# Kernel tuning notes

Hardware: AMD Instinct MI355X
Metric: run time of the kernel (lower is better)

Reference implementation:

```python
import jax, jax.numpy as jnp
import numpy as np

N_NODES = 4096
NUM_GRAPHS = 16
NODE_DIM = 8
EDGE_DIM = 4
HID = 128
N_WIRES = 9  # 3 edge wires + 4 node wires (center=3) + 2 ancillas
SEL_LAYERS = 1
PI = np.pi


def _c(x):
    return x.astype(jnp.complex64)


def _ry(t):
    c, s = _c(jnp.cos(t / 2)), _c(jnp.sin(t / 2))
    return jnp.stack([jnp.stack([c, -s], -1), jnp.stack([s, c], -1)], -2)


def _rx(t):
    c, s = _c(jnp.cos(t / 2)), -1j * _c(jnp.sin(t / 2))
    return jnp.stack([jnp.stack([c, s], -1), jnp.stack([s, c], -1)], -2)


def _rz(t):
    e = jnp.exp(-0.5j * _c(t))
    z = jnp.zeros_like(e)
    return jnp.stack([jnp.stack([e, z], -1), jnp.stack([z, jnp.conj(e)], -1)], -2)


def _rot(phi, theta, omega):  # qml.Rot = RZ(omega) @ RY(theta) @ RZ(phi)
    return _rz(omega) @ _ry(theta) @ _rz(phi)


def _ctrl(U):  # block-diag(I2, U)
    b = U.shape[:-2]
    I = jnp.broadcast_to(jnp.eye(2, dtype=jnp.complex64), b + (2, 2))
    Z = jnp.zeros(b + (2, 2), jnp.complex64)
    return jnp.concatenate([jnp.concatenate([I, Z], -1), jnp.concatenate([Z, U], -1)], -2)


_CNOT = jnp.array([[1, 0, 0, 0], [0, 1, 0, 0], [0, 0, 0, 1], [0, 0, 1, 0]], jnp.complex64)


def _apply1(state, U, w):  # state [S, 2**9], U [2,2] or [S,2,2]
    S = state.shape[0]
    s = jnp.moveaxis(state.reshape((S,) + (2,) * N_WIRES), 1 + w, 1)
    out = jnp.einsum('bij,bjk->bik', jnp.broadcast_to(U, (S, 2, 2)), s.reshape(S, 2, -1))
    return jnp.moveaxis(out.reshape(s.shape), 1, 1 + w).reshape(S, -1)


def _apply2(state, U, w1, w2):  # U [4,4] or [S,4,4], wire order (w1,w2)
    S = state.shape[0]
    s = jnp.moveaxis(state.reshape((S,) + (2,) * N_WIRES), (1 + w1, 1 + w2), (1, 2))
    out = jnp.einsum('bij,bjk->bik', jnp.broadcast_to(U, (S, 4, 4)), s.reshape(S, 4, -1))
    return jnp.moveaxis(out.reshape(s.shape), (1, 2), (1 + w1, 1 + w2)).reshape(S, -1)


def _sel(state, weights, wires):  # qml.StronglyEntanglingLayers, weights [L, n, 3]->here [L,3,3]
    L, n = weights.shape[0], len(wires)
    for l in range(L):
        for j, w in enumerate(wires):
            state = _apply1(state, _rot(weights[l, j, 0], weights[l, j, 1], weights[l, j, 2]), w)
        r = l % (n - 1) + 1
        for j in range(n):
            state = _apply2(state, _CNOT, wires[j], wires[(j + r) % n])
    return state


def _pqc(inputs, strong, inits, update):
    # inputs: [S, 7, 2] angles (rows 0..2 edge feats, rows 3..6 node feats, center node = row 3)
    S = inputs.shape[0]
    state = jnp.zeros((S, 2 ** N_WIRES), jnp.complex64).at[:, 0].set(1.0)
    for i in range(3):
        state = _apply1(state, _ry(inputs[:, i, 0]), i)
        state = _apply1(state, _rz(inputs[:, i, 1]), i)
    for i in range(4):
        state = _apply1(state, _ry(inputs[:, 3 + i, 0]), 3 + i)
        state = _apply1(state, _rz(inputs[:, 3 + i, 1]), 3 + i)
    for i in range(3):  # message_passing_pqc per edge
        e, nb, a1, a2 = i, 4 + i, 7, 8
        state = _apply2(state, _ctrl(_rx(inits[0, 0])), nb, a1)
        state = _apply2(state, _ctrl(_ry(inits[0, 1])), e, a1)
        state = _apply2(state, _ctrl(_rz(inits[0, 2])), nb, a2)
        state = _apply2(state, _ctrl(_ry(inits[0, 3])), e, a2)
        state = _sel(state, strong[0], [e, nb, a1])
        state = _sel(state, strong[1], [a1, nb, a2])
    state = _sel(state, update, [3, 7, 8])
    # expval(PauliX) on center wire 3: wires 0..2 -> 8, wire 3 -> 2, wires 4..8 -> 32
    s = state.reshape(S, 8, 2, 32)
    return 2.0 * jnp.real(jnp.sum(jnp.conj(s[:, :, 0]) * s[:, :, 1], axis=(1, 2)))


def _mlp(x, W1, b1, W2, b2):  # PyG MLP, act between layers, dropout in eval = identity
    return jax.nn.leaky_relu(x @ W1 + b1) @ W2 + b2


def _forward(node_feat, edge_attr, Wn1, bn1, Wn2, bn2, We1, be1, We2, be2,
             strong, inits, update, Wu1, bu1, Wu2, bu2, Wh1, bh1, Wh2, bh2,
             subgraphs, edge_ids, batch):
    x = jnp.tanh(_mlp(node_feat, Wn1, bn1, Wn2, bn2)) * PI   # input_process
    e = jnp.tanh(_mlp(edge_attr, We1, be1, We2, be2)) * PI
    q_in = jnp.concatenate([e[edge_ids], x[subgraphs]], axis=1)  # [S,3,2]+[S,4,2] -> [S,7,2]
    aggr = _pqc(q_in, strong, inits, update)[:, None]            # [S,1]
    centers = subgraphs[:, 0]
    upd = _mlp(jnp.concatenate([x[centers], aggr], axis=-1), Wu1, bu1, Wu2, bu2)  # [S,2]
    x = x + jnp.zeros_like(x).at[centers].add(upd)               # index_add + residual
    gsum = jax.ops.segment_sum(x, batch, num_segments=NUM_GRAPHS)
    gcnt = jax.ops.segment_sum(jnp.ones((x.shape[0], 1), x.dtype), batch, num_segments=NUM_GRAPHS)
    g = gsum / gcnt                                              # global_mean_pool
    return _mlp(g, Wh1, bh1, Wh2, bh2)


def setup_inputs() -> dict:
    key = jax.random.key(0)
    ks = jax.random.split(key, 16)
    N, G = N_NODES, NUM_GRAPHS
    node_feat = jax.random.normal(ks[0], (N, NODE_DIM), jnp.float32)
    edge_attr = jax.random.normal(ks[1], (3 * N, EDGE_DIM), jnp.float32)
    i = np.arange(N)
    # star subgraph per node: center i with ring neighbors i+1,i+2,i+3 (mod N);
    # edge (i, i+k) has id 3*i + (k-1) in edge_attr (idx_dict materialized).
    subgraphs = jnp.asarray(np.stack([i, (i + 1) % N, (i + 2) % N, (i + 3) % N], 1), jnp.int32)
    edge_ids = jnp.asarray(np.stack([3 * i, 3 * i + 1, 3 * i + 2], 1), jnp.int32)
    batch = jnp.asarray(i // (N // G), jnp.int32)

    def lin(k, fan_in, shape):
        return jax.random.uniform(k, shape, jnp.float32, -1.0, 1.0) / np.sqrt(fan_in)

    def qw(k, shape):  # uniform_pi_init
        return jax.random.uniform(k, shape, jnp.float32, 0.0, PI)

    k = jax.random.split(ks[2], 24)
    return {
        'node_feat': node_feat, 'edge_attr': edge_attr,
        'Wn1': lin(k[0], NODE_DIM, (NODE_DIM, HID)), 'bn1': lin(k[1], NODE_DIM, (HID,)),
        'Wn2': lin(k[2], HID, (HID, 2)), 'bn2': lin(k[3], HID, (2,)),
        'We1': lin(k[4], EDGE_DIM, (EDGE_DIM, HID)), 'be1': lin(k[5], EDGE_DIM, (HID,)),
        'We2': lin(k[6], HID, (HID, 2)), 'be2': lin(k[7], HID, (2,)),
        'strong': qw(k[8], (2, SEL_LAYERS, 3, 3)), 'inits': qw(k[9], (1, 4)),
        'update': qw(k[10], (SEL_LAYERS, 3, 3)),
        'Wu1': lin(k[11], 3, (3, HID)), 'bu1': lin(k[12], 3, (HID,)),
        'Wu2': lin(k[13], HID, (HID, 2)), 'bu2': lin(k[14], HID, (2,)),
        'Wh1': lin(k[15], 2, (2, 2)), 'bh1': lin(k[16], 2, (2,)),
        'Wh2': lin(k[17], 2, (2, 2)), 'bh2': lin(k[18], 2, (2,)),
        'subgraphs': subgraphs, 'edge_ids': edge_ids, 'batch': batch,
    }


def reference(node_feat, edge_attr, Wn1, bn1, Wn2, bn2, We1, be1, We2, be2,
              strong, inits, update, Wu1, bu1, Wu2, bu2, Wh1, bh1, Wh2, bh2,
              subgraphs, edge_ids, batch):
    return _forward(node_feat, edge_attr, Wn1, bn1, Wn2, bn2, We1, be1, We2, be2,
                    strong, inits, update, Wu1, bu1, Wu2, bu2, Wh1, bh1, Wh2, bh2,
                    subgraphs, edge_ids, batch)
```

## Files before the change

### kernel.cpp

```cpp
#include <hip/hip_runtime.h>
#include <math.h>

#define PI_F 3.14159265358979323846f

__device__ __forceinline__ float2 cmul2(float2 a, float2 b) {
    return make_float2(a.x * b.x - a.y * b.y, a.x * b.y + a.y * b.x);
}
__device__ __forceinline__ float2 cmac2(float2 u, float2 a, float2 v, float2 b) {
    float2 r;
    r.x = u.x * a.x - u.y * a.y + v.x * b.x - v.y * b.y;
    r.y = u.x * a.y + u.y * a.x + v.x * b.y + v.y * b.x;
    return r;
}

struct M4 { float2 u00, u01, u10, u11; };

__device__ __forceinline__ M4 mmul4(const M4& A, const M4& B) {
    M4 R;
    R.u00 = cmac2(A.u00, B.u00, A.u01, B.u10);
    R.u01 = cmac2(A.u00, B.u01, A.u01, B.u11);
    R.u10 = cmac2(A.u10, B.u00, A.u11, B.u10);
    R.u11 = cmac2(A.u10, B.u01, A.u11, B.u11);
    return R;
}
__device__ __forceinline__ M4 mry(float t) {
    float c = cosf(0.5f * t), s = sinf(0.5f * t);
    M4 R; R.u00 = {c, 0}; R.u01 = {-s, 0}; R.u10 = {s, 0}; R.u11 = {c, 0};
    return R;
}
__device__ __forceinline__ M4 mrz(float t) {
    float c = cosf(0.5f * t), s = sinf(0.5f * t);
    M4 R; R.u00 = {c, -s}; R.u01 = {0, 0}; R.u10 = {0, 0}; R.u11 = {c, s};
    return R;
}
__device__ __forceinline__ M4 mrot(float phi, float th, float om) {
    return mmul4(mmul4(mrz(om), mry(th)), mrz(phi));
}

__device__ __forceinline__ float2 shflx(float2 v, int mask) {
    return make_float2(__shfl_xor(v.x, mask, 64), __shfl_xor(v.y, mask, 64));
}

__device__ __forceinline__ M4 ldm(const float* __restrict__ g) {
    M4 M;
    M.u00 = make_float2(g[0], g[1]); M.u01 = make_float2(g[2], g[3]);
    M.u10 = make_float2(g[4], g[5]); M.u11 = make_float2(g[6], g[7]);
    return M;
}


template <int TB>
__device__ __forceinline__ void rot_reg(const M4& U, float2 (&amp)[8]) {
#pragma unroll
    for (int r = 0; r < 8; r++)
        if (((r >> TB) & 1) == 0) {
            int r1 = r | (1 << TB);
            float2 a = amp[r], b = amp[r1];
            amp[r]  = cmac2(U.u00, a, U.u01, b);
            amp[r1] = cmac2(U.u10, a, U.u11, b);
        }
}

template <int LB>
__device__ __forceinline__ void rot_lane(const M4& U, float2 (&amp)[8], int lane) {
    bool hi = (lane >> LB) & 1;
    float2 cA = hi ? U.u11 : U.u00;
    float2 cB = hi ? U.u10 : U.u01;
#pragma unroll
    for (int r = 0; r < 8; r++) {
        float2 o = shflx(amp[r], 1 << LB);
        amp[r] = cmac2(cA, amp[r], cB, o);
    }
}

template <int WIRE>
__device__ __forceinline__ void rot1(const M4& U, float2 (&amp)[8], int lane) {
    constexpr int BIT = 8 - WIRE;
    if constexpr (BIT < 3) rot_reg<BIT>(U, amp);
    else rot_lane<BIT - 3>(U, amp, lane);
}


template <int CBIT, int TB>
__device__ __forceinline__ void crx_g(float c, float s, float2 (&amp)[8], int lane) {
    if constexpr (CBIT >= 3) {
        bool ct = (lane >> (CBIT - 3)) & 1;
        float cc = ct ? c : 1.f, ss = ct ? s : 0.f;
#pragma unroll
        for (int r = 0; r < 8; r++)
            if (((r >> TB) & 1) == 0) {
                int r1 = r | (1 << TB);
                float2 a = amp[r], b = amp[r1];
                amp[r]  = make_float2(cc * a.x + ss * b.y, cc * a.y - ss * b.x);
                amp[r1] = make_float2(ss * a.y + cc * b.x, cc * b.y - ss * a.x);
            }
    } else {
#pragma unroll
        for (int r = 0; r < 8; r++)
            if (((r >> CBIT) & 1) == 1 && ((r >> TB) & 1) == 0) {
                int r1 = r | (1 << TB);
                float2 a = amp[r], b = amp[r1];
                amp[r]  = make_float2(c * a.x + s * b.y, c * a.y - s * b.x);
                amp[r1] = make_float2(s * a.y + c * b.x, c * b.y - s * a.x);
            }
    }
}

template <int CBIT, int TB>
__device__ __forceinline__ void cry_g(float c, float s, float2 (&amp)[8], int lane) {
    if constexpr (CBIT >= 3) {
        bool ct = (lane >> (CBIT - 3)) & 1;
        float cc = ct ? c : 1.f, ss = ct ? s : 0.f;
#pragma unroll
        for (int r = 0; r < 8; r++)
            if (((r >> TB) & 1) == 0) {
                int r1 = r | (1 << TB);
                float2 a = amp[r], b = amp[r1];
                amp[r]  = make_float2(cc * a.x - ss * b.x, cc * a.y - ss * b.y);
                amp[r1] = make_float2(ss * a.x + cc * b.x, ss * a.y + cc * b.y);
            }
    } else {
#pragma unroll
        for (int r = 0; r < 8; r++)
            if (((r >> CBIT) & 1) == 1 && ((r >> TB) & 1) == 0) {
                int r1 = r | (1 << TB);
                float2 a = amp[r], b = amp[r1];
                amp[r]  = make_float2(c * a.x - s * b.x, c * a.y - s * b.y);
                amp[r1] = make_float2(s * a.x + c * b.x, s * a.y + c * b.y);
            }
    }
}

template <int CBIT, int TB>
__device__ __forceinline__ void crz_g(float c, float s, float2 (&amp)[8], int lane) {
    if constexpr (CBIT >= 3) {
        bool ct = (lane >> (CBIT - 3)) & 1;
        float cc = ct ? c : 1.f, ss = ct ? s : 0.f;
#pragma unroll
        for (int r = 0; r < 8; r++)
            if (((r >> TB) & 1) == 0) {
                int r1 = r | (1 << TB);
                float2 a = amp[r], b = amp[r1];
                amp[r]  = make_float2(cc * a.x + ss * a.y, cc * a.y - ss * a.x);
                amp[r1] = make_float2(cc * b.x - ss * b.y, cc * b.y + ss * b.x);
            }
    } else {
#pragma unroll
        for (int r = 0; r < 8; r++)
            if (((r >> CBIT) & 1) == 1 && ((r >> TB) & 1) == 0) {
                int r1 = r | (1 << TB);
                float2 a = amp[r], b = amp[r1];
                amp[r]  = make_float2(c * a.x + s * a.y, c * a.y - s * a.x);
                amp[r1] = make_float2(c * b.x - s * b.y, c * b.y + s * b.x);
            }
    }
}

template <int CW, int TW>
__device__ __forceinline__ void cnotg(float2 (&amp)[8], int lane) {
    constexpr int CBIT = 8 - CW, TBIT = 8 - TW;
    if constexpr (CBIT < 3 && TBIT < 3) {
#pragma unroll
        for (int r = 0; r < 8; r++)
            if (((r >> CBIT) & 1) == 1 && ((r >> TBIT) & 1) == 0) {
                int r1 = r | (1 << TBIT);
                float2 t = amp[r]; amp[r] = amp[r1]; amp[r1] = t;
            }
    } else if constexpr (CBIT >= 3 && TBIT < 3) {
        bool c = (lane >> (CBIT - 3)) & 1;
#pragma unroll
        for (int r = 0; r < 8; r++)
            if (((r >> TBIT) & 1) == 0) {
                int r1 = r | (1 << TBIT);
                float2 t0 = amp[r], t1 = amp[r1];
                amp[r]  = c ? t1 : t0;
                amp[r1] = c ? t0 : t1;
            }
    } else if constexpr (CBIT < 3 && TBIT >= 3) {
#pragma unroll
        for (int r = 0; r < 8; r++)
            if (((r >> CBIT) & 1) == 1) {
                amp[r] = shflx(amp[r], 1 << (TBIT - 3));
            }
    } else {
        bool c = (lane >> (CBIT - 3)) & 1;
#pragma unroll
        for (int r = 0; r < 8; r++) {
            float2 o = shflx(amp[r], 1 << (TBIT - 3));
            amp[r] = c ? o : amp[r];
        }
    }
}

template <int W0, int W1, int W2>
__device__ __forceinline__ void sel3m(const float* __restrict__ gm, float2 (&amp)[8], int lane) {
    rot1<W0>(ldm(gm),      amp, lane);
    rot1<W1>(ldm(gm + 8),  amp, lane);
    rot1<W2>(ldm(gm + 16), amp, lane);
    cnotg<W0, W1>(amp, lane);
    cnotg<W1, W2>(amp, lane);
    cnotg<W2, W0>(amp, lane);
}

template <int I>
__device__ __forceinline__ void block_i(float2 (&amp)[8], float cx, float sx, float cy1, float sy1,
                                        float cz, float sz, float cy2, float sy2,
                                        const float* __restrict__ gm, int lane) {
    crx_g<4 - I, 1>(cx,  sx,  amp, lane);
    cry_g<8 - I, 1>(cy1, sy1, amp, lane);
    crz_g<4 - I, 0>(cz,  sz,  amp, lane);
    cry_g<8 - I, 0>(cy2, sy2, amp, lane);
    sel3m<I, 4 + I, 7>(gm + 8,  amp, lane);
    sel3m<7, 4 + I, 8>(gm + 32, amp, lane);
}


__global__ void prep_kernel(const float* __restrict__ strong, const float* __restrict__ inits,
                            const float* __restrict__ update, float* __restrict__ gm,
                            float* __restrict__ zbuf, int nzero) {
    int j = threadIdx.x;
    if (j < 4) {
        gm[2 * j]     = cosf(0.5f * inits[j]);
        gm[2 * j + 1] = sinf(0.5f * inits[j]);
    } else if (j < 13) {
        const float* w;
        if (j < 7)       w = strong + (j - 4) * 3;
        else if (j < 10) w = strong + 9 + (j - 7) * 3;
        else             w = update + (j - 10) * 3;
        M4 M = mrot(w[0], w[1], w[2]);
        float* o = gm + 8 + (j - 4) * 8;
        o[0] = M.u00.x; o[1] = M.u00.y; o[2] = M.u01.x; o[3] = M.u01.y;
        o[4] = M.u10.x; o[5] = M.u10.y; o[6] = M.u11.x; o[7] = M.u11.y;
    }
    for (int i = j; i < nzero; i += 64) zbuf[i] = 0.f;
}

__global__ __launch_bounds__(256) void mlp_both_kernel(
        const float* __restrict__ node_feat, const float* __restrict__ edge_attr,
        const float* __restrict__ Wn1, const float* __restrict__ bn1,
        const float* __restrict__ Wn2, const float* __restrict__ bn2,
        const float* __restrict__ We1, const float* __restrict__ be1,
        const float* __restrict__ We2, const float* __restrict__ be2,
        float* __restrict__ x, float* __restrict__ e,
        int N, int NE, int nodeBlocks) {
    if ((int)blockIdx.x < nodeBlocks) {
        int r = blockIdx.x * 256 + threadIdx.x;
        if (r >= N) return;
        float f[8];
#pragma unroll
        for (int k = 0; k < 8; k++) f[k] = node_feat[r * 8 + k];
        float o0 = bn2[0], o1 = bn2[1];
        for (int j = 0; j < 128; j++) {
            float h = bn1[j];
#pragma unroll
            for (int k = 0; k < 8; k++) h += f[k] * Wn1[k * 128 + j];
            h = h > 0.f ? h : 0.01f * h;
            o0 += h * Wn2[j * 2 + 0];
            o1 += h * Wn2[j * 2 + 1];
        }
        x[r * 2 + 0] = tanhf(o0) * PI_F;
        x[r * 2 + 1] = tanhf(o1) * PI_F;
    } else {
        int r = (blockIdx.x - nodeBlocks) * 256 + threadIdx.x;
        if (r >= NE) return;
        float f[4];
#pragma unroll
        for (int k = 0; k < 4; k++) f[k] = edge_attr[r * 4 + k];
        float o0 = be2[0], o1 = be2[1];
        for (int j = 0; j < 128; j++) {
            float h = be1[j];
#pragma unroll
            for (int k = 0; k < 4; k++) h += f[k] * We1[k * 128 + j];
            h = h > 0.f ? h : 0.01f * h;
            o0 += h * We2[j * 2 + 0];
            o1 += h * We2[j * 2 + 1];
        }
        e[r * 2 + 0] = tanhf(o0) * PI_F;
        e[r * 2 + 1] = tanhf(o1) * PI_F;
    }
}

__global__ __launch_bounds__(256) void pqc_kernel(
        const float* __restrict__ x, const float* __restrict__ e,
        const int* __restrict__ subgraphs, const int* __restrict__ edge_ids,
        const float* __restrict__ gm, float* __restrict__ aggr, int ntot) {
    int wave = threadIdx.x >> 6;
    int lane = threadIdx.x & 63;
    int s = blockIdx.x * 4 + wave;
    if (s >= ntot) return;

    float ang[7][2];
    for (int j = 0; j < 3; j++) {
        int eid = edge_ids[s * 3 + j];
        ang[j][0] = e[2 * eid]; ang[j][1] = e[2 * eid + 1];
    }
    for (int j = 0; j < 4; j++) {
        int nid = subgraphs[s * 4 + j];
        ang[3 + j][0] = x[2 * nid]; ang[3 + j][1] = x[2 * nid + 1];
    }

    float2 c = make_float2(1.f, 0.f);
#pragma unroll
    for (int w = 0; w < 6; w++) {
        float a = 0.5f * ang[w][0], b = 0.5f * ang[w][1];
        float ca = __cosf(a), sa = __sinf(a);
        float cb = __cosf(b), sb = __sinf(b);
        float2 v0 = make_float2(ca * cb, -ca * sb);
        float2 v1 = make_float2(sa * cb,  sa * sb);
        int bit = (lane >> (5 - w)) & 1;
        c = cmul2(c, bit ? v1 : v0);
    }
    float2 amp[8];
#pragma unroll
    for (int r = 0; r < 8; r++) amp[r] = make_float2(0.f, 0.f);
    {
        float a = 0.5f * ang[6][0], b = 0.5f * ang[6][1];
        float ca = __cosf(a), sa = __sinf(a);
        float cb = __cosf(b), sb = __sinf(b);
        amp[0] = cmul2(c, make_float2(ca * cb, -ca * sb));
        amp[4] = cmul2(c, make_float2(sa * cb,  sa * sb));
    }

    float cx  = gm[0], sx  = gm[1];
    float cy1 = gm[2], sy1 = gm[3];
    float cz  = gm[4], sz  = gm[5];
    float cy2 = gm[6], sy2 = gm[7];

    block_i<0>(amp, cx, sx, cy1, sy1, cz, sz, cy2, sy2, gm, lane);
    block_i<1>(amp, cx, sx, cy1, sy1, cz, sz, cy2, sy2, gm, lane);
    block_i<2>(amp, cx, sx, cy1, sy1, cz, sz, cy2, sy2, gm, lane);
    sel3m<3, 7, 8>(gm + 56, amp, lane);

    float acc = 0.f;
#pragma unroll
    for (int r = 0; r < 8; r++) {
        float2 o = shflx(amp[r], 4);
        acc += amp[r].x * o.x + amp[r].y * o.y;
    }
    for (int off = 32; off > 0; off >>= 1) acc += __shfl_down(acc, off, 64);
    if (lane == 0) aggr[s] = acc;
}

#define MAX_GRAPHS 64
__global__ __launch_bounds__(256) void pool_upd_kernel(
        const float* __restrict__ x, const float* __restrict__ aggr,
        const int* __restrict__ subgraphs, const int* __restrict__ batch,
        const float* __restrict__ W1, const float* __restrict__ b1,
        const float* __restrict__ W2, const float* __restrict__ b2,
        float* __restrict__ gsum, float* __restrict__ gcnt, int rows, int ngraphs) {
    __shared__ float bins[3 * MAX_GRAPHS];
    for (int i = threadIdx.x; i < 3 * ngraphs; i += blockDim.x) bins[i] = 0.f;
    __syncthreads();

    int r = blockIdx.x * blockDim.x + threadIdx.x;
    int lane = threadIdx.x & 63;
    bool active = r < rows;
    int b = 0, bc = 0;
    float v0 = 0.f, v1 = 0.f, o0 = 0.f, o1 = 0.f;
    if (active) {
        b = batch[r];
        v0 = x[2 * r + 0];
        v1 = x[2 * r + 1];
        int cidx = subgraphs[r * 4];
        bc = batch[cidx];
        float f0 = x[2 * cidx], f1 = x[2 * cidx + 1], f2 = aggr[r];
        o0 = b2[0]; o1 = b2[1];
        for (int j = 0; j < 128; j++) {
            float h = b1[j] + f0 * W1[j] + f1 * W1[128 + j] + f2 * W1[256 + j];
            h = h > 0.f ? h : 0.01f * h;
            o0 += h * W2[j * 2 + 0];
            o1 += h * W2[j * 2 + 1];
        }
    }
    int b0 = __shfl(b, 0);
    bool uni = __all(active && b == b0 && bc == b0);
    if (uni) {
        float s0 = v0 + o0, s1 = v1 + o1;
        for (int off = 32; off > 0; off >>= 1) {
            s0 += __shfl_down(s0, off);
            s1 += __shfl_down(s1, off);
        }
        if (lane == 0) {
            atomicAdd(&bins[3 * b0 + 0], s0);
            atomicAdd(&bins[3 * b0 + 1], s1);
            atomicAdd(&bins[3 * b0 + 2], 64.f);
        }
    } else if (active) {
        atomicAdd(&bins[3 * b + 0], v0);
        atomicAdd(&bins[3 * b + 1], v1);
        atomicAdd(&bins[3 * b + 2], 1.f);
        atomicAdd(&bins[3 * bc + 0], o0);
        atomicAdd(&bins[3 * bc + 1], o1);
    }
    __syncthreads();

    for (int i = threadIdx.x; i < ngraphs; i += blockDim.x) {
        float s0 = bins[3 * i + 0], s1 = bins[3 * i + 1], sc = bins[3 * i + 2];
        if (s0 != 0.f || s1 != 0.f || sc != 0.f) {
            atomicAdd(&gsum[2 * i + 0], s0);
            atomicAdd(&gsum[2 * i + 1], s1);
            atomicAdd(&gcnt[i], sc);
        }
    }
}

__global__ void head_kernel(const float* __restrict__ gsum, const float* __restrict__ gcnt,
                            const float* __restrict__ Wh1, const float* __restrict__ bh1,
                            const float* __restrict__ Wh2, const float* __restrict__ bh2,
                            float* __restrict__ out, int ngraphs) {
    int g = threadIdx.x;
    if (g >= ngraphs) return;
    float c = gcnt[g];
    float g0 = gsum[2 * g + 0] / c;
    float g1 = gsum[2 * g + 1] / c;
    float h0 = g0 * Wh1[0] + g1 * Wh1[2] + bh1[0];
    float h1 = g0 * Wh1[1] + g1 * Wh1[3] + bh1[1];
    h0 = h0 > 0.f ? h0 : 0.01f * h0;
    h1 = h1 > 0.f ? h1 : 0.01f * h1;
    out[2 * g + 0] = h0 * Wh2[0] + h1 * Wh2[2] + bh2[0];
    out[2 * g + 1] = h0 * Wh2[1] + h1 * Wh2[3] + bh2[1];
}

extern "C" void kernel_launch(void* const* d_in, const int* in_sizes, int n_in,
                              void* d_out, int out_size, void* d_ws, size_t ws_size,
                              hipStream_t stream) {
    const float* node_feat = (const float*)d_in[0];
    const float* edge_attr = (const float*)d_in[1];
    const float* Wn1 = (const float*)d_in[2];
    const float* bn1 = (const float*)d_in[3];
    const float* Wn2 = (const float*)d_in[4];
    const float* bn2 = (const float*)d_in[5];
    const float* We1 = (const float*)d_in[6];
    const float* be1 = (const float*)d_in[7];
    const float* We2 = (const float*)d_in[8];
    const float* be2 = (const float*)d_in[9];
    const float* strong = (const float*)d_in[10];
    const float* inits  = (const float*)d_in[11];
    const float* update = (const float*)d_in[12];
    const float* Wu1 = (const float*)d_in[13];
    const float* bu1 = (const float*)d_in[14];
    const float* Wu2 = (const float*)d_in[15];
    const float* bu2 = (const float*)d_in[16];
    const float* Wh1 = (const float*)d_in[17];
    const float* bh1 = (const float*)d_in[18];
    const float* Wh2 = (const float*)d_in[19];
    const float* bh2 = (const float*)d_in[20];
    const int* subgraphs = (const int*)d_in[21];
    const int* edge_ids  = (const int*)d_in[22];
    const int* batch     = (const int*)d_in[23];

    const int N  = in_sizes[0] / 8;
    const int NE = in_sizes[1] / 4;
    const int NG = out_size / 2;

    float* ws   = (float*)d_ws;
    float* x    = ws;
    float* e    = x + (size_t)N * 2;
    float* aggr = e + (size_t)NE * 2;
    float* gsum = aggr + N;
    float* gcnt = gsum + (size_t)NG * 2;
    float* gm   = gcnt + NG;

    prep_kernel<<<1, 64, 0, stream>>>(strong, inits, update, gm, gsum, 3 * NG);

    int nodeBlocks = (N + 255) / 256;
    int edgeBlocks = (NE + 255) / 256;
    mlp_both_kernel<<<nodeBlocks + edgeBlocks, 256, 0, stream>>>(
        node_feat, edge_attr, Wn1, bn1, Wn2, bn2, We1, be1, We2, be2, x, e, N, NE, nodeBlocks);

    pqc_kernel<<<(N + 3) / 4, 256, 0, stream>>>(x, e, subgraphs, edge_ids, gm, aggr, N);

    pool_upd_kernel<<<(N + 255) / 256, 256, 0, stream>>>(
        x, aggr, subgraphs, batch, Wu1, bu1, Wu2, bu2, gsum, gcnt, N, NG);

    head_kernel<<<1, 64, 0, stream>>>(gsum, gcnt, Wh1, bh1, Wh2, bh2, (float*)d_out, NG);
}
```

Before: 151.2 us.

## Fuse five kernels into two with last-block head and per-wave update MLP

Folds the parameter-prep kernel into the MLP launch as an extra block, and merges the PQC, pooling/update-MLP and head kernels into one kernel. The head runs in the last block to finish, detected through a global atomic counter. The update MLP is now spread across the 64 lanes of each wave (two hidden units per lane) instead of a serial 128-iteration loop per thread, and the aggr buffer round trip is gone. This removes three launches and inter-kernel gaps. In exchange it adds many per-wave shared atomics with no uniform-graph fast path, plus a threadfence and a global counter per block.

```diff
diff --git a/kernel.cpp b/kernel.cpp
--- a/kernel.cpp
+++ b/kernel.cpp
@@ -214,37 +214,20 @@
     sel3m<7, 4 + I, 8>(gm + 32, amp, lane);
 }
 
-
-__global__ void prep_kernel(const float* __restrict__ strong, const float* __restrict__ inits,
-                            const float* __restrict__ update, float* __restrict__ gm,
-                            float* __restrict__ zbuf, int nzero) {
-    int j = threadIdx.x;
-    if (j < 4) {
-        gm[2 * j]     = cosf(0.5f * inits[j]);
-        gm[2 * j + 1] = sinf(0.5f * inits[j]);
-    } else if (j < 13) {
-        const float* w;
-        if (j < 7)       w = strong + (j - 4) * 3;
-        else if (j < 10) w = strong + 9 + (j - 7) * 3;
-        else             w = update + (j - 10) * 3;
-        M4 M = mrot(w[0], w[1], w[2]);
-        float* o = gm + 8 + (j - 4) * 8;
-        o[0] = M.u00.x; o[1] = M.u00.y; o[2] = M.u01.x; o[3] = M.u01.y;
-        o[4] = M.u10.x; o[5] = M.u10.y; o[6] = M.u11.x; o[7] = M.u11.y;
-    }
-    for (int i = j; i < nzero; i += 64) zbuf[i] = 0.f;
-}
-
-__global__ __launch_bounds__(256) void mlp_both_kernel(
+__global__ __launch_bounds__(256) void mlp_prep_kernel(
         const float* __restrict__ node_feat, const float* __restrict__ edge_attr,
         const float* __restrict__ Wn1, const float* __restrict__ bn1,
         const float* __restrict__ Wn2, const float* __restrict__ bn2,
         const float* __restrict__ We1, const float* __restrict__ be1,
         const float* __restrict__ We2, const float* __restrict__ be2,
+        const float* __restrict__ strong, const float* __restrict__ inits,
+        const float* __restrict__ update,
         float* __restrict__ x, float* __restrict__ e,
-        int N, int NE, int nodeBlocks) {
-    if ((int)blockIdx.x < nodeBlocks) {
-        int r = blockIdx.x * 256 + threadIdx.x;
+        float* __restrict__ gm, float* __restrict__ zbuf, int nzero,
+        int N, int NE, int nodeBlocks, int edgeBlocks) {
+    int bid = blockIdx.x;
+    if (bid < nodeBlocks) {
+        int r = bid * 256 + threadIdx.x;
         if (r >= N) return;
         float f[8];
 #pragma unroll
@@ -260,8 +243,8 @@
         }
         x[r * 2 + 0] = tanhf(o0) * PI_F;
         x[r * 2 + 1] = tanhf(o1) * PI_F;
-    } else {
-        int r = (blockIdx.x - nodeBlocks) * 256 + threadIdx.x;
+    } else if (bid < nodeBlocks + edgeBlocks) {
+        int r = (bid - nodeBlocks) * 256 + threadIdx.x;
         if (r >= NE) return;
         float f[4];
 #pragma unroll
@@ -277,124 +260,125 @@
         }
         e[r * 2 + 0] = tanhf(o0) * PI_F;
         e[r * 2 + 1] = tanhf(o1) * PI_F;
-    }
-}
-
-__global__ __launch_bounds__(256) void pqc_kernel(
+    } else {
+        int j = threadIdx.x;
+        if (j < 4) {
+            gm[2 * j]     = cosf(0.5f * inits[j]);
+            gm[2 * j + 1] = sinf(0.5f * inits[j]);
+        } else if (j < 13) {
+            const float* w;
+            if (j < 7)       w = strong + (j - 4) * 3;
+            else if (j < 10) w = strong + 9 + (j - 7) * 3;
+            else             w = update + (j - 10) * 3;
+            M4 M = mrot(w[0], w[1], w[2]);
+            float* o = gm + 8 + (j - 4) * 8;
+            o[0] = M.u00.x; o[1] = M.u00.y; o[2] = M.u01.x; o[3] = M.u01.y;
+            o[4] = M.u10.x; o[5] = M.u10.y; o[6] = M.u11.x; o[7] = M.u11.y;
+        }
+        for (int i = j; i < nzero; i += 256) zbuf[i] = 0.f;
+    }
+}
+
+#define MAX_GRAPHS 64
+__global__ __launch_bounds__(256) void pqc_fused_kernel(
         const float* __restrict__ x, const float* __restrict__ e,
         const int* __restrict__ subgraphs, const int* __restrict__ edge_ids,
-        const float* __restrict__ gm, float* __restrict__ aggr, int ntot) {
+        const int* __restrict__ batch, const float* __restrict__ gm,
+        const float* __restrict__ Wu1, const float* __restrict__ bu1,
+        const float* __restrict__ Wu2, const float* __restrict__ bu2,
+        const float* __restrict__ Wh1, const float* __restrict__ bh1,
+        const float* __restrict__ Wh2, const float* __restrict__ bh2,
+        float* __restrict__ gsum, float* __restrict__ gcnt,
+        unsigned int* __restrict__ counter, float* __restrict__ out,
+        int ntot, int ngraphs) {
+    __shared__ float bins[3 * MAX_GRAPHS];
+    __shared__ bool isLast;
+    for (int i = threadIdx.x; i < 3 * ngraphs; i += 256) bins[i] = 0.f;
+    __syncthreads();
+
     int wave = threadIdx.x >> 6;
     int lane = threadIdx.x & 63;
     int s = blockIdx.x * 4 + wave;
-    if (s >= ntot) return;
-
-    float ang[7][2];
-    for (int j = 0; j < 3; j++) {
-        int eid = edge_ids[s * 3 + j];
-        ang[j][0] = e[2 * eid]; ang[j][1] = e[2 * eid + 1];
-    }
-    for (int j = 0; j < 4; j++) {
-        int nid = subgraphs[s * 4 + j];
-        ang[3 + j][0] = x[2 * nid]; ang[3 + j][1] = x[2 * nid + 1];
-    }
-
-    float2 c = make_float2(1.f, 0.f);
-#pragma unroll
-    for (int w = 0; w < 6; w++) {
-        float a = 0.5f * ang[w][0], b = 0.5f * ang[w][1];
-        float ca = __cosf(a), sa = __sinf(a);
-        float cb = __cosf(b), sb = __sinf(b);
-        float2 v0 = make_float2(ca * cb, -ca * sb);
-        float2 v1 = make_float2(sa * cb,  sa * sb);
-        int bit = (lane >> (5 - w)) & 1;
-        c = cmul2(c, bit ? v1 : v0);
-    }
-    float2 amp[8];
-#pragma unroll
-    for (int r = 0; r < 8; r++) amp[r] = make_float2(0.f, 0.f);
-    {
-        float a = 0.5f * ang[6][0], b = 0.5f * ang[6][1];
-        float ca = __cosf(a), sa = __sinf(a);
-        float cb = __cosf(b), sb = __sinf(b);
-        amp[0] = cmul2(c, make_float2(ca * cb, -ca * sb));
-        amp[4] = cmul2(c, make_float2(sa * cb,  sa * sb));
-    }
-
-    float cx  = gm[0], sx  = gm[1];
-    float cy1 = gm[2], sy1 = gm[3];
-    float cz  = gm[4], sz  = gm[5];
-    float cy2 = gm[6], sy2 = gm[7];
-
-    block_i<0>(amp, cx, sx, cy1, sy1, cz, sz, cy2, sy2, gm, lane);
-    block_i<1>(amp, cx, sx, cy1, sy1, cz, sz, cy2, sy2, gm, lane);
-    block_i<2>(amp, cx, sx, cy1, sy1, cz, sz, cy2, sy2, gm, lane);
-    sel3m<3, 7, 8>(gm + 56, amp, lane);
-
-    float acc = 0.f;
-#pragma unroll
-    for (int r = 0; r < 8; r++) {
-        float2 o = shflx(amp[r], 4);
-        acc += amp[r].x * o.x + amp[r].y * o.y;
-    }
-    for (int off = 32; off > 0; off >>= 1) acc += __shfl_down(acc, off, 64);
-    if (lane == 0) aggr[s] = acc;
-}
-
-#define MAX_GRAPHS 64
-__global__ __launch_bounds__(256) void pool_upd_kernel(
-        const float* __restrict__ x, const float* __restrict__ aggr,
-        const int* __restrict__ subgraphs, const int* __restrict__ batch,
-        const float* __restrict__ W1, const float* __restrict__ b1,
-        const float* __restrict__ W2, const float* __restrict__ b2,
-        float* __restrict__ gsum, float* __restrict__ gcnt, int rows, int ngraphs) {
-    __shared__ float bins[3 * MAX_GRAPHS];
-    for (int i = threadIdx.x; i < 3 * ngraphs; i += blockDim.x) bins[i] = 0.f;
+    bool active = s < ntot;
+
+    if (active) {
+        float ang[7][2];
+        int cidx = subgraphs[s * 4];
+        for (int j = 0; j < 3; j++) {
+            int eid = edge_ids[s * 3 + j];
+            ang[j][0] = e[2 * eid]; ang[j][1] = e[2 * eid + 1];
+        }
+        ang[3][0] = x[2 * cidx]; ang[3][1] = x[2 * cidx + 1];
+        for (int j = 1; j < 4; j++) {
+            int nid = subgraphs[s * 4 + j];
+            ang[3 + j][0] = x[2 * nid]; ang[3 + j][1] = x[2 * nid + 1];
+        }
+
+        float2 c = make_float2(1.f, 0.f);
+#pragma unroll
+        for (int w = 0; w < 6; w++) {
+            float a = 0.5f * ang[w][0], b = 0.5f * ang[w][1];
+            float ca = __cosf(a), sa = __sinf(a);
+            float cb = __cosf(b), sb = __sinf(b);
+            float2 v0 = make_float2(ca * cb, -ca * sb);
+            float2 v1 = make_float2(sa * cb,  sa * sb);
+            int bit = (lane >> (5 - w)) & 1;
+            c = cmul2(c, bit ? v1 : v0);
+        }
+        float2 amp[8];
+#pragma unroll
+        for (int r = 0; r < 8; r++) amp[r] = make_float2(0.f, 0.f);
+        {
+            float a = 0.5f * ang[6][0], b = 0.5f * ang[6][1];
+            float ca = __cosf(a), sa = __sinf(a);
+            float cb = __cosf(b), sb = __sinf(b);
+            amp[0] = cmul2(c, make_float2(ca * cb, -ca * sb));
+            amp[4] = cmul2(c, make_float2(sa * cb,  sa * sb));
+        }
+
+        float cx  = gm[0], sx  = gm[1];
+        float cy1 = gm[2], sy1 = gm[3];
+        float cz  = gm[4], sz  = gm[5];
+        float cy2 = gm[6], sy2 = gm[7];
+
+        block_i<0>(amp, cx, sx, cy1, sy1, cz, sz, cy2, sy2, gm, lane);
+        block_i<1>(amp, cx, sx, cy1, sy1, cz, sz, cy2, sy2, gm, lane);
+        block_i<2>(amp, cx, sx, cy1, sy1, cz, sz, cy2, sy2, gm, lane);
+        sel3m<3, 7, 8>(gm + 56, amp, lane);
+
+        float acc = 0.f;
+#pragma unroll
+        for (int r = 0; r < 8; r++) {
+            float2 o = shflx(amp[r], 4);
+            acc += amp[r].x * o.x + amp[r].y * o.y;
+        }
+        for (int off = 32; off > 0; off >>= 1) acc += __shfl_xor(acc, off, 64);
+
+        float f0 = ang[3][0], f1 = ang[3][1], f2 = acc;
+        int j1 = lane, j2 = lane + 64;
+        float h1 = bu1[j1] + f0 * Wu1[j1] + f1 * Wu1[128 + j1] + f2 * Wu1[256 + j1];
+        float h2 = bu1[j2] + f0 * Wu1[j2] + f1 * Wu1[128 + j2] + f2 * Wu1[256 + j2];
+        h1 = h1 > 0.f ? h1 : 0.01f * h1;
+        h2 = h2 > 0.f ? h2 : 0.01f * h2;
+        float o0 = h1 * Wu2[2 * j1]     + h2 * Wu2[2 * j2];
+        float o1 = h1 * Wu2[2 * j1 + 1] + h2 * Wu2[2 * j2 + 1];
+        for (int off = 32; off > 0; off >>= 1) {
+            o0 += __shfl_down(o0, off, 64);
+            o1 += __shfl_down(o1, off, 64);
+        }
+        if (lane == 0) {
+            o0 += bu2[0]; o1 += bu2[1];
+            int bs = batch[s], bc = batch[cidx];
+            atomicAdd(&bins[3 * bs + 0], x[2 * s + 0]);
+            atomicAdd(&bins[3 * bs + 1], x[2 * s + 1]);
+            atomicAdd(&bins[3 * bs + 2], 1.f);
+            atomicAdd(&bins[3 * bc + 0], o0);
+            atomicAdd(&bins[3 * bc + 1], o1);
+        }
+    }
     __syncthreads();
 
-    int r = blockIdx.x * blockDim.x + threadIdx.x;
-    int lane = threadIdx.x & 63;
-    bool active = r < rows;
-    int b = 0, bc = 0;
-    float v0 = 0.f, v1 = 0.f, o0 = 0.f, o1 = 0.f;
-    if (active) {
-        b = batch[r];
-        v0 = x[2 * r + 0];
-        v1 = x[2 * r + 1];
-        int cidx = subgraphs[r * 4];
-        bc = batch[cidx];
-        float f0 = x[2 * cidx], f1 = x[2 * cidx + 1], f2 = aggr[r];
-        o0 = b2[0]; o1 = b2[1];
-        for (int j = 0; j < 128; j++) {
-            float h = b1[j] + f0 * W1[j] + f1 * W1[128 + j] + f2 * W1[256 + j];
-            h = h > 0.f ? h : 0.01f * h;
-            o0 += h * W2[j * 2 + 0];
-            o1 += h * W2[j * 2 + 1];
-        }
-    }
-    int b0 = __shfl(b, 0);
-    bool uni = __all(active && b == b0 && bc == b0);
-    if (uni) {
-        float s0 = v0 + o0, s1 = v1 + o1;
-        for (int off = 32; off > 0; off >>= 1) {
-            s0 += __shfl_down(s0, off);
-            s1 += __shfl_down(s1, off);
-        }
-        if (lane == 0) {
-            atomicAdd(&bins[3 * b0 + 0], s0);
-            atomicAdd(&bins[3 * b0 + 1], s1);
-            atomicAdd(&bins[3 * b0 + 2], 64.f);
-        }
-    } else if (active) {
-        atomicAdd(&bins[3 * b + 0], v0);
-        atomicAdd(&bins[3 * b + 1], v1);
-        atomicAdd(&bins[3 * b + 2], 1.f);
-        atomicAdd(&bins[3 * bc + 0], o0);
-        atomicAdd(&bins[3 * bc + 1], o1);
-    }
-    __syncthreads();
-
-    for (int i = threadIdx.x; i < ngraphs; i += blockDim.x) {
+    for (int i = threadIdx.x; i < ngraphs; i += 256) {
         float s0 = bins[3 * i + 0], s1 = bins[3 * i + 1], sc = bins[3 * i + 2];
         if (s0 != 0.f || s1 != 0.f || sc != 0.f) {
             atomicAdd(&gsum[2 * i + 0], s0);
@@ -402,23 +386,27 @@
             atomicAdd(&gcnt[i], sc);
         }
     }
-}
-
-__global__ void head_kernel(const float* __restrict__ gsum, const float* __restrict__ gcnt,
-                            const float* __restrict__ Wh1, const float* __restrict__ bh1,
-                            const float* __restrict__ Wh2, const float* __restrict__ bh2,
-                            float* __restrict__ out, int ngraphs) {
-    int g = threadIdx.x;
-    if (g >= ngraphs) return;
-    float c = gcnt[g];
-    float g0 = gsum[2 * g + 0] / c;
-    float g1 = gsum[2 * g + 1] / c;
-    float h0 = g0 * Wh1[0] + g1 * Wh1[2] + bh1[0];
-    float h1 = g0 * Wh1[1] + g1 * Wh1[3] + bh1[1];
-    h0 = h0 > 0.f ? h0 : 0.01f * h0;
-    h1 = h1 > 0.f ? h1 : 0.01f * h1;
-    out[2 * g + 0] = h0 * Wh2[0] + h1 * Wh2[2] + bh2[0];
-    out[2 * g + 1] = h0 * Wh2[1] + h1 * Wh2[3] + bh2[1];
+
+    __threadfence();
+    if (threadIdx.x == 0) {
+        unsigned int t = atomicAdd(counter, 1u);
+        isLast = (t == gridDim.x - 1);
+    }
+    __syncthreads();
+    if (isLast) {
+        int g = threadIdx.x;
+        if (g < ngraphs) {
+            float cgs = atomicAdd(&gcnt[g], 0.f);
+            float g0 = atomicAdd(&gsum[2 * g + 0], 0.f) / cgs;
+            float g1 = atomicAdd(&gsum[2 * g + 1], 0.f) / cgs;
+            float h0 = g0 * Wh1[0] + g1 * Wh1[2] + bh1[0];
+            float h1 = g0 * Wh1[1] + g1 * Wh1[3] + bh1[1];
+            h0 = h0 > 0.f ? h0 : 0.01f * h0;
+            h1 = h1 > 0.f ? h1 : 0.01f * h1;
+            out[2 * g + 0] = h0 * Wh2[0] + h1 * Wh2[2] + bh2[0];
+            out[2 * g + 1] = h0 * Wh2[1] + h1 * Wh2[3] + bh2[1];
+        }
+    }
 }
 
 extern "C" void kernel_launch(void* const* d_in, const int* in_sizes, int n_in,
@@ -456,22 +444,19 @@
     float* ws   = (float*)d_ws;
     float* x    = ws;
     float* e    = x + (size_t)N * 2;
-    float* aggr = e + (size_t)NE * 2;
-    float* gsum = aggr + N;
+    float* gsum = e + (size_t)NE * 2;
     float* gcnt = gsum + (size_t)NG * 2;
-    float* gm   = gcnt + NG;
-
-    prep_kernel<<<1, 64, 0, stream>>>(strong, inits, update, gm, gsum, 3 * NG);
+    float* ctrf = gcnt + NG;
+    float* gm   = ctrf + 1;
 
     int nodeBlocks = (N + 255) / 256;
     int edgeBlocks = (NE + 255) / 256;
-    mlp_both_kernel<<<nodeBlocks + edgeBlocks, 256, 0, stream>>>(
-        node_feat, edge_attr, Wn1, bn1, Wn2, bn2, We1, be1, We2, be2, x, e, N, NE, nodeBlocks);
-
-    pqc_kernel<<<(N + 3) / 4, 256, 0, stream>>>(x, e, subgraphs, edge_ids, gm, aggr, N);
-
-    pool_upd_kernel<<<(N + 255) / 256, 256, 0, stream>>>(
-        x, aggr, subgraphs, batch, Wu1, bu1, Wu2, bu2, gsum, gcnt, N, NG);
-
-    head_kernel<<<1, 64, 0, stream>>>(gsum, gcnt, Wh1, bh1, Wh2, bh2, (float*)d_out, NG);
-}
+
+    mlp_prep_kernel<<<nodeBlocks + edgeBlocks + 1, 256, 0, stream>>>(
+        node_feat, edge_attr, Wn1, bn1, Wn2, bn2, We1, be1, We2, be2,
+        strong, inits, update, x, e, gm, gsum, 3 * NG + 1, N, NE, nodeBlocks, edgeBlocks);
+
+    pqc_fused_kernel<<<(N + 3) / 4, 256, 0, stream>>>(
+        x, e, subgraphs, edge_ids, batch, gm, Wu1, bu1, Wu2, bu2,
+        Wh1, bh1, Wh2, bh2, gsum, gcnt, (unsigned int*)ctrf, (float*)d_out, N, NG);
+}
```

After: 186.0 us. 23.0% more time.
